# Kernel optimization log

Measured on AMD Instinct MI355X. Metric: run time of the kernel, lower is better.

The kernel has to match this reference:

```python
import jax, jax.numpy as jnp
import numpy as np

N_CELL, N_WELL = 200000, 2000
E_CC, E_CW = 1200000, 200000
CF, WF, H = 16, 8, 128
NUM_PHASES, OUT_SEQ = 3, 25
OUT = NUM_PHASES * OUT_SEQ  # 75


def setup_inputs() -> dict:
    key = jax.random.key(0)
    ks = jax.random.split(key, 24)
    p = lambda k, shp: jax.random.normal(k, shp, dtype=jnp.float32) * 0.02
    return {
        "cell_x": jax.random.normal(ks[0], (N_CELL, CF), dtype=jnp.float32),
        "well_x": jax.random.normal(ks[1], (N_WELL, WF), dtype=jnp.float32),
        "edge_index_cell": jax.random.randint(ks[2], (2, E_CC), 0, N_CELL),
        "edge_well_src": jax.random.randint(ks[3], (E_CW,), 0, N_CELL),
        "edge_well_dst": jax.random.randint(ks[4], (E_CW,), 0, N_WELL),
        # input projections
        "W_cell": p(ks[5], (CF, H)), "b_cell": jnp.zeros((H,), jnp.float32),
        "W_well": p(ks[6], (WF, H)), "b_well": jnp.zeros((H,), jnp.float32),
        # SAGEConv cell->cell: lin_l (on aggregated neighbors, has bias), lin_r (on root, no bias)
        "Wl_cc": p(ks[7], (H, H)), "bl_cc": jnp.zeros((H,), jnp.float32),
        "Wr_cc": p(ks[8], (H, H)),
        # SAGEConv cell->well (bipartite)
        "Wl_cw": p(ks[9], (H, H)), "bl_cw": jnp.zeros((H,), jnp.float32),
        "Wr_cw": p(ks[10], (H, H)),
        # well MLP
        "W_m1": p(ks[11], (H, H)), "b_m1": jnp.zeros((H,), jnp.float32),
        "W_m2": p(ks[12], (H, OUT)), "b_m2": jnp.zeros((OUT,), jnp.float32),
    }


def _mean_aggr(msgs, dst, num_segments):
    # PyG 'mean' aggregation: sum per destination / neighbor count; 0 for isolated nodes.
    s = jax.ops.segment_sum(msgs, dst, num_segments=num_segments)
    c = jax.ops.segment_sum(jnp.ones((dst.shape[0], 1), msgs.dtype), dst, num_segments=num_segments)
    return s / jnp.maximum(c, 1.0)


def reference(cell_x, well_x, edge_index_cell, edge_well_src, edge_well_dst,
              W_cell, b_cell, W_well, b_well,
              Wl_cc, bl_cc, Wr_cc, Wl_cw, bl_cw, Wr_cw,
              W_m1, b_m1, W_m2, b_m2):
    cell_h = cell_x @ W_cell + b_cell                      # [N_cell, H]
    well_h = well_x @ W_well + b_well                      # [N_well, H]

    # SAGEConv(cell_h, edge_index_cell): gather source feats, mean-scatter to dst
    src, dst = edge_index_cell[0], edge_index_cell[1]
    agg_c = _mean_aggr(cell_h[src], dst, N_CELL)           # [N_cell, H]
    cell_h = agg_c @ Wl_cc + bl_cc + cell_h @ Wr_cc

    # Bipartite SAGEConv((cell_h, well_h), edge_well): aggregate cells into wells
    agg_w = _mean_aggr(cell_h[edge_well_src], edge_well_dst, N_WELL)  # [N_well, H]
    well_h = agg_w @ Wl_cw + bl_cw + well_h @ Wr_cw

    # well MLP head
    h = jax.nn.relu(well_h @ W_m1 + b_m1)
    out = h @ W_m2 + b_m2                                  # [N_well, 75]
    return out.reshape(-1, NUM_PHASES, OUT_SEQ)            # [N_well, 3, 25]
```

## Files before the change

### kernel.cpp

```cpp
#include <hip/hip_runtime.h>

#define N_CELL 200000
#define N_WELL 2000
#define E_CC   1200000
#define E_CW   200000
#define CF     16
#define WF     8
#define H      128
#define OUTF   75

#define CAP_C  16
#define CAP_W  224
#define OVF_CAP 16384
#define WPB    4

#define BLD_T  307200
#define MKW_T  50176

__device__ __forceinline__ float b2f(unsigned short u) {
    union { unsigned int i; float f; } v; v.i = ((unsigned int)u) << 16; return v.f;
}
__device__ __forceinline__ unsigned short f2b(float f) {
    union { float f; unsigned int i; } v; v.f = f;
    unsigned int i = v.i;
    return (unsigned short)((i + 0x7fffu + ((i >> 16) & 1u)) >> 16);
}
__device__ __forceinline__ float lo16(unsigned int v) { return b2f((unsigned short)(v & 0xffffu)); }
__device__ __forceinline__ float hi16(unsigned int v) { return b2f((unsigned short)(v >> 16)); }
__device__ __forceinline__ float ldf(const void* p, int i, int bf) {
    return bf ? b2f(((const unsigned short*)p)[i]) : ((const float*)p)[i];
}

__global__ __launch_bounds__(256) void k_sniff(const unsigned int* __restrict__ x, int* __restrict__ flag)
{
    __shared__ int cnt[256];
    int t = threadIdx.x;
    unsigned int d = x[t];
    unsigned int e = (d >> 7) & 0xffu;
    cnt[t] = (e >= 110u && e <= 135u) ? 1 : 0;
    __syncthreads();
    for (int o = 128; o > 0; o >>= 1) { if (t < o) cnt[t] += cnt[t + o]; __syncthreads(); }
    if (t == 0) flag[0] = (cnt[0] >= 192) ? 1 : 0;
}

__global__ __launch_bounds__(128) void k_precomp(const void* __restrict__ W_cell,
                                                 const void* __restrict__ b_cell,
                                                 const void* __restrict__ Wl,
                                                 const void* __restrict__ Wr,
                                                 const void* __restrict__ bl,
                                                 const int* __restrict__ flag,
                                                 float* __restrict__ G1, float* __restrict__ G2,
                                                 float* __restrict__ g1v, float* __restrict__ g2v)
{
    int f = threadIdx.x, b = blockIdx.x, bf = flag[0];
    if (b < 16) {
        float s1 = 0.f, s2 = 0.f;
        for (int j = 0; j < H; ++j) {
            float wc = ldf(W_cell, b * H + j, bf);
            s1 += wc * ldf(Wl, j * H + f, bf);
            s2 += wc * ldf(Wr, j * H + f, bf);
        }
        G1[b * H + f] = s1; G2[b * H + f] = s2;
    } else {
        float s1 = 0.f, s2 = 0.f;
        for (int j = 0; j < H; ++j) {
            float bc = ldf(b_cell, j, bf);
            s1 += bc * ldf(Wl, j * H + f, bf);
            s2 += bc * ldf(Wr, j * H + f, bf);
        }
        g1v[f] = s1; g2v[f] = s2 + ldf(bl, f, bf);
    }
}

__global__ __launch_bounds__(128) void k_precomp2(const float* __restrict__ G1, const float* __restrict__ G2,
                                                  const float* __restrict__ g1v, const float* __restrict__ g2v,
                                                  const void* __restrict__ Wl_cw,
                                                  const void* __restrict__ bl_cw,
                                                  const void* __restrict__ Wr_cw,
                                                  const void* __restrict__ W_well,
                                                  const void* __restrict__ b_well,
                                                  const void* __restrict__ Wm1, const void* __restrict__ Wm2,
                                                  const void* __restrict__ bm1, const void* __restrict__ bm2,
                                                  const int* __restrict__ flag,
                                                  float* __restrict__ A1, float* __restrict__ A2,
                                                  float* __restrict__ Bm,
                                                  float* __restrict__ a1, float* __restrict__ a2,
                                                  float* __restrict__ b0,
                                                  float* __restrict__ Wm1f, float* __restrict__ Wm2f,
                                                  float* __restrict__ bm1f, float* __restrict__ bm2f)
{
    int f = threadIdx.x, b = blockIdx.x, bf = flag[0];
    if (b < 16) {
        float s1 = 0.f, s2 = 0.f;
        for (int j = 0; j < H; ++j) {
            float wl = ldf(Wl_cw, j * H + f, bf);
            s1 += G1[b * H + j] * wl;
            s2 += G2[b * H + j] * wl;
        }
        A1[b * H + f] = s1; A2[b * H + f] = s2;
    } else if (b < 24) {
        int k = b - 16;
        float s = 0.f;
        for (int j = 0; j < H; ++j)
            s += ldf(W_well, k * H + j, bf) * ldf(Wr_cw, j * H + f, bf);
        Bm[k * H + f] = s;
    } else if (b == 24) {
        float s1 = 0.f, s2 = 0.f, s3 = 0.f;
        for (int j = 0; j < H; ++j) {
            float wl = ldf(Wl_cw, j * H + f, bf);
            s1 += g1v[j] * wl;
            s2 += g2v[j] * wl;
            s3 += ldf(b_well, j, bf) * ldf(Wr_cw, j * H + f, bf);
        }
        a1[f] = s1; a2[f] = s2; b0[f] = s3 + ldf(bl_cw, f, bf);
    } else {
        int i = (b - 25) * 128 + f;
        if (i < H * H) Wm1f[i] = ldf(Wm1, i, bf);
        else if (i < H * H + H * OUTF) Wm2f[i - H * H] = ldf(Wm2, i - H * H, bf);
        else if (i < H * H + H * OUTF + H) bm1f[i - H * H - H * OUTF] = ldf(bm1, i - H * H - H * OUTF, bf);
        else if (i < H * H + H * OUTF + H + OUTF) bm2f[i - H * H - H * OUTF - H] = ldf(bm2, i - H * H - H * OUTF - H, bf);
    }
}

__global__ __launch_bounds__(256) void k_markw(const int* __restrict__ ews, const int* __restrict__ ewd,
                                               unsigned char* __restrict__ mark,
                                               int* __restrict__ counts_w, int* __restrict__ buckets_w)
{
    int i = blockIdx.x * 256 + threadIdx.x;
#pragma unroll
    for (int u = 0; u < 4; ++u) {
        int e = i + u * MKW_T;
        if (e < E_CW) {
            unsigned c = (unsigned)ews[e];
            if (c < N_CELL) mark[c] = 1;
            unsigned d = (unsigned)ewd[e];
            if (d < N_WELL) {
                int s = atomicAdd(&counts_w[d], 1);
                if (s < CAP_W) buckets_w[d * CAP_W + s] = (int)c;
            }
        }
    }
}

__global__ __launch_bounds__(256) void k_build(const int* __restrict__ cc_src, const int* __restrict__ cc_dst,
                                               const unsigned char* __restrict__ mark,
                                               int* __restrict__ counts_c,
                                               int* __restrict__ buckets_c,
                                               int* __restrict__ ovf_cnt, int2* __restrict__ ovf)
{
    int i = blockIdx.x * 256 + threadIdx.x;
    int e0 = i, e1 = i + BLD_T, e2 = i + 2 * BLD_T, e3 = i + 3 * BLD_T;
    unsigned d0 = (e0 < E_CC) ? (unsigned)cc_dst[e0] : 0xFFFFFFFFu;
    unsigned d1 = (e1 < E_CC) ? (unsigned)cc_dst[e1] : 0xFFFFFFFFu;
    unsigned d2 = (e2 < E_CC) ? (unsigned)cc_dst[e2] : 0xFFFFFFFFu;
    unsigned d3 = (e3 < E_CC) ? (unsigned)cc_dst[e3] : 0xFFFFFFFFu;
    bool m0 = (d0 < N_CELL) && mark[d0];
    bool m1 = (d1 < N_CELL) && mark[d1];
    bool m2 = (d2 < N_CELL) && mark[d2];
    bool m3 = (d3 < N_CELL) && mark[d3];
    int s0 = m0 ? cc_src[e0] : 0;
    int s1 = m1 ? cc_src[e1] : 0;
    int s2 = m2 ? cc_src[e2] : 0;
    int s3 = m3 ? cc_src[e3] : 0;
    if (m0) {
        int p = atomicAdd(&counts_c[d0], 1);
        if (p < CAP_C) buckets_c[d0 * CAP_C + p] = s0;
        else { int q = atomicAdd(ovf_cnt, 1); if (q < OVF_CAP) { ovf[q].x = (int)d0; ovf[q].y = s0; } }
    }
    if (m1) {
        int p = atomicAdd(&counts_c[d1], 1);
        if (p < CAP_C) buckets_c[d1 * CAP_C + p] = s1;
        else { int q = atomicAdd(ovf_cnt, 1); if (q < OVF_CAP) { ovf[q].x = (int)d1; ovf[q].y = s1; } }
    }
    if (m2) {
        int p = atomicAdd(&counts_c[d2], 1);
        if (p < CAP_C) buckets_c[d2 * CAP_C + p] = s2;
        else { int q = atomicAdd(ovf_cnt, 1); if (q < OVF_CAP) { ovf[q].x = (int)d2; ovf[q].y = s2; } }
    }
    if (m3) {
        int p = atomicAdd(&counts_c[d3], 1);
        if (p < CAP_C) buckets_c[d3 * CAP_C + p] = s3;
        else { int q = atomicAdd(ovf_cnt, 1); if (q < OVF_CAP) { ovf[q].x = (int)d3; ovf[q].y = s3; } }
    }
}

__global__ __launch_bounds__(256) void k_aggA(const void* __restrict__ xr,
                                              const int* __restrict__ flag,
                                              const unsigned char* __restrict__ mark,
                                              const int* __restrict__ counts_c,
                                              const int* __restrict__ buckets_c,
                                              float* __restrict__ y)
{
    int gid = (blockIdx.x * 256 + threadIdx.x) >> 3;
    int jl = threadIdx.x & 7;
    if (gid >= N_CELL) return;
    if (!mark[gid]) return;
    int bf = flag[0];
    int cnt = counts_c[gid]; if (cnt < 0) cnt = 0;
    int lim = (cnt < CAP_C) ? cnt : CAP_C;
    float acc[16];
#pragma unroll
    for (int k = 0; k < 16; ++k) acc[k] = 0.f;

    int j0 = jl, j1 = jl + 8;
    unsigned s0 = (j0 < lim) ? (unsigned)buckets_c[gid * CAP_C + j0] : 0xFFFFFFFFu;
    unsigned s1 = (j1 < lim) ? (unsigned)buckets_c[gid * CAP_C + j1] : 0xFFFFFFFFu;
    if (s0 >= N_CELL) s0 = 0xFFFFFFFFu;
    if (s1 >= N_CELL) s1 = 0xFFFFFFFFu;

    if (bf) {
        uint4 a0, b0q, a1, b1q;
        bool v0 = (s0 != 0xFFFFFFFFu), v1 = (s1 != 0xFFFFFFFFu);
        if (v0) { a0 = ((const uint4*)xr)[(size_t)s0 * 2]; b0q = ((const uint4*)xr)[(size_t)s0 * 2 + 1]; }
        if (v1) { a1 = ((const uint4*)xr)[(size_t)s1 * 2]; b1q = ((const uint4*)xr)[(size_t)s1 * 2 + 1]; }
        if (v0) {
            acc[0] += lo16(a0.x);  acc[1] += hi16(a0.x);
            acc[2] += lo16(a0.y);  acc[3] += hi16(a0.y);
            acc[4] += lo16(a0.z);  acc[5] += hi16(a0.z);
            acc[6] += lo16(a0.w);  acc[7] += hi16(a0.w);
            acc[8] += lo16(b0q.x); acc[9] += hi16(b0q.x);
            acc[10] += lo16(b0q.y); acc[11] += hi16(b0q.y);
            acc[12] += lo16(b0q.z); acc[13] += hi16(b0q.z);
            acc[14] += lo16(b0q.w); acc[15] += hi16(b0q.w);
        }
        if (v1) {
            acc[0] += lo16(a1.x);  acc[1] += hi16(a1.x);
            acc[2] += lo16(a1.y);  acc[3] += hi16(a1.y);
            acc[4] += lo16(a1.z);  acc[5] += hi16(a1.z);
            acc[6] += lo16(a1.w);  acc[7] += hi16(a1.w);
            acc[8] += lo16(b1q.x); acc[9] += hi16(b1q.x);
            acc[10] += lo16(b1q.y); acc[11] += hi16(b1q.y);
            acc[12] += lo16(b1q.z); acc[13] += hi16(b1q.z);
            acc[14] += lo16(b1q.w); acc[15] += hi16(b1q.w);
        }
    } else {
        if (s0 != 0xFFFFFFFFu) {
            const float4* p = (const float4*)xr + (size_t)s0 * 4;
#pragma unroll
            for (int q = 0; q < 4; ++q) {
                float4 v = p[q];
                acc[4 * q] += v.x; acc[4 * q + 1] += v.y; acc[4 * q + 2] += v.z; acc[4 * q + 3] += v.w;
            }
        }
        if (s1 != 0xFFFFFFFFu) {
            const float4* p = (const float4*)xr + (size_t)s1 * 4;
#pragma unroll
            for (int q = 0; q < 4; ++q) {
                float4 v = p[q];
                acc[4 * q] += v.x; acc[4 * q + 1] += v.y; acc[4 * q + 2] += v.z; acc[4 * q + 3] += v.w;
            }
        }
    }
#pragma unroll
    for (int m = 1; m < 8; m <<= 1) {
#pragma unroll
        for (int k = 0; k < 16; ++k) acc[k] += __shfl_xor(acc[k], m, 64);
    }
    float sc = (cnt > 0) ? (1.0f / (float)cnt) : 0.0f;
    float2 st; st.x = acc[2 * jl] * sc; st.y = acc[2 * jl + 1] * sc;
    ((float2*)y)[(size_t)gid * 8 + jl] = st;
}

__global__ __launch_bounds__(256) void k_ovf(const void* __restrict__ xr,
                                             const int* __restrict__ flag,
                                             const int* __restrict__ ovf_cnt,
                                             const int2* __restrict__ ovf,
                                             const int* __restrict__ counts_c,
                                             float* __restrict__ y)
{
    int gid = (blockIdx.x * 256 + threadIdx.x) >> 3;
    int jl = threadIdx.x & 7;
    int n = ovf_cnt[0]; if (n > OVF_CAP) n = OVF_CAP;
    if (gid >= n) return;
    int bf = flag[0];
    unsigned d = (unsigned)ovf[gid].x; if (d >= N_CELL) d = 0;
    unsigned s = (unsigned)ovf[gid].y; if (s >= N_CELL) s = 0;
    int cnt = counts_c[d];
    float inv = (cnt > 0) ? (1.0f / (float)cnt) : 0.0f;
    float v0, v1;
    if (bf) {
        unsigned int u = ((const unsigned int*)xr)[(size_t)s * 8 + jl];
        v0 = lo16(u); v1 = hi16(u);
    } else {
        v0 = ((const float*)xr)[(size_t)s * 16 + 2 * jl];
        v1 = ((const float*)xr)[(size_t)s * 16 + 2 * jl + 1];
    }
    atomicAdd(&y[(size_t)d * 16 + 2 * jl], v0 * inv);
    atomicAdd(&y[(size_t)d * 16 + 2 * jl + 1], v1 * inv);
}

__global__ __launch_bounds__(256) void k_wellagg(const void* __restrict__ xr,
                                                 const int* __restrict__ flag,
                                                 const float* __restrict__ y,
                                                 const int* __restrict__ counts_c,
                                                 const int* __restrict__ counts_w,
                                                 const int* __restrict__ buckets_w,
                                                 const void* __restrict__ wx,
                                                 const float* __restrict__ A1, const float* __restrict__ A2,
                                                 const float* __restrict__ Bm,
                                                 const float* __restrict__ a1, const float* __restrict__ a2,
                                                 const float* __restrict__ b0,
                                                 float* __restrict__ Z)
{
    __shared__ float sP[16], sR[16], sq[1];
    int w = blockIdx.x, t = threadIdx.x, bf = flag[0];
    int g = t >> 3, jl = t & 7;
    if (t < 16) { sP[t] = 0.f; sR[t] = 0.f; }
    if (t == 16) sq[0] = 0.f;
    __syncthreads();

    int cntw = counts_w[w]; if (cntw < 0) cntw = 0;
    int lim = (cntw < CAP_W) ? cntw : CAP_W;

    float p0 = 0.f, p1 = 0.f, r0 = 0.f, r1 = 0.f, qn = 0.f;
    const unsigned int* x32 = (const unsigned int*)xr;
    const float* xf = (const float*)xr;

    for (int e = g; e < lim; e += 32) {
        unsigned c = (unsigned)buckets_w[w * CAP_W + e]; if (c >= N_CELL) c = 0;
        float2 yv = ((const float2*)y)[(size_t)c * 8 + jl];
        p0 += yv.x; p1 += yv.y;
        if (bf) {
            unsigned int u = x32[(size_t)c * 8 + jl];
            r0 += lo16(u); r1 += hi16(u);
        } else {
            r0 += xf[(size_t)c * 16 + 2 * jl];
            r1 += xf[(size_t)c * 16 + 2 * jl + 1];
        }
        if (jl == 0) qn += (counts_c[c] > 0) ? 1.0f : 0.0f;
    }
    atomicAdd(&sP[2 * jl], p0);
    atomicAdd(&sP[2 * jl + 1], p1);
    atomicAdd(&sR[2 * jl], r0);
    atomicAdd(&sR[2 * jl + 1], r1);
    if (jl == 0 && qn != 0.f) atomicAdd(&sq[0], qn);
    __syncthreads();

    int f = t;
    if (f < H) {
        float inv = (cntw > 0) ? (1.0f / (float)cntw) : 0.0f;
        float mask = (cntw > 0) ? 1.0f : 0.0f;
        float wh = (sq[0] * inv) * a1[f] + a2[f];
#pragma unroll
        for (int k = 0; k < 16; ++k)
            wh += (sP[k] * inv) * A1[k * H + f] + (sR[k] * inv) * A2[k * H + f];
        wh *= mask;
        wh += b0[f];
#pragma unroll
        for (int k = 0; k < WF; ++k)
            wh += ldf(wx, w * WF + k, bf) * Bm[k * H + f];
        Z[(size_t)w * H + f] = wh;
    }
}

__global__ __launch_bounds__(128) void k_head(const float* __restrict__ Z,
                                              const float* __restrict__ Wm1f, const float* __restrict__ Wm2f,
                                              const float* __restrict__ bm1f, const float* __restrict__ bm2f,
                                              const int* __restrict__ flag,
                                              void* __restrict__ outp)
{
    __shared__ float sz[WPB][H], sh[WPB][H];
    int w0 = blockIdx.x * WPB, t = threadIdx.x, bf = flag[0];
    float4 zv = ((const float4*)(Z + (size_t)w0 * H))[t];
    ((float4*)&sz[0][0])[t] = zv;
    __syncthreads();

    float acc[WPB];
#pragma unroll
    for (int i = 0; i < WPB; ++i) acc[i] = bm1f[t];
    for (int k = 0; k < H; ++k) {
        float wm = Wm1f[k * H + t];
#pragma unroll
        for (int i = 0; i < WPB; ++i) acc[i] += sz[i][k] * wm;
    }
#pragma unroll
    for (int i = 0; i < WPB; ++i) sh[i][t] = fmaxf(acc[i], 0.f);
    __syncthreads();

    if (t < OUTF) {
        float o[WPB];
#pragma unroll
        for (int i = 0; i < WPB; ++i) o[i] = bm2f[t];
        for (int k = 0; k < H; ++k) {
            float wm = Wm2f[k * OUTF + t];
#pragma unroll
            for (int i = 0; i < WPB; ++i) o[i] += sh[i][k] * wm;
        }
        if (bf) {
#pragma unroll
            for (int i = 0; i < WPB; ++i)
                ((unsigned short*)outp)[(size_t)(w0 + i) * OUTF + t] = f2b(o[i]);
        } else {
#pragma unroll
            for (int i = 0; i < WPB; ++i)
                ((float*)outp)[(size_t)(w0 + i) * OUTF + t] = o[i];
        }
    }
}

extern "C" void kernel_launch(void* const* d_in, const int* in_sizes, int n_in,
                              void* d_out, int out_size, void* d_ws, size_t ws_size,
                              hipStream_t stream)
{
    const void* cell_x = d_in[0];
    const void* well_x = d_in[1];
    const int* eic = (const int*)d_in[2];
    const int* ews = (const int*)d_in[3];
    const int* ewd = (const int*)d_in[4];
    const void* W_cell = d_in[5];
    const void* b_cell = d_in[6];
    const void* W_well = d_in[7];
    const void* b_well = d_in[8];
    const void* Wl_cc = d_in[9];
    const void* bl_cc = d_in[10];
    const void* Wr_cc = d_in[11];
    const void* Wl_cw = d_in[12];
    const void* bl_cw = d_in[13];
    const void* Wr_cw = d_in[14];
    const void* W_m1 = d_in[15];
    const void* b_m1 = d_in[16];
    const void* W_m2 = d_in[17];
    const void* b_m2 = d_in[18];
    (void)in_sizes; (void)n_in; (void)out_size; (void)ws_size;

    const int* cc_src = eic;
    const int* cc_dst = eic + E_CC;

    char* wsp = (char*)d_ws;
    size_t off = 0;
    auto carve = [&](size_t bytes) -> char* {
        char* p = wsp + off;
        off = (off + bytes + 255) & ~(size_t)255;
        return p;
    };

    float* G1   = (float*)carve(16 * H * 4);
    float* G2   = (float*)carve(16 * H * 4);
    float* g1v  = (float*)carve(H * 4);
    float* g2v  = (float*)carve(H * 4);
    float* A1   = (float*)carve(16 * H * 4);
    float* A2   = (float*)carve(16 * H * 4);
    float* Bm   = (float*)carve(WF * H * 4);
    float* a1   = (float*)carve(H * 4);
    float* a2   = (float*)carve(H * 4);
    float* b0   = (float*)carve(H * 4);
    float* Wm1f = (float*)carve(H * H * 4);
    float* Wm2f = (float*)carve(H * OUTF * 4);
    float* bm1f = (float*)carve(H * 4);
    float* bm2f = (float*)carve(OUTF * 4);
    int*   flag = (int*)carve(256);
    size_t zero_beg = off;
    int*   counts   = (int*)carve((size_t)(N_CELL + N_WELL) * 4);
    int*   counts_c = counts;
    int*   counts_w = counts + N_CELL;
    unsigned char* mark = (unsigned char*)carve((size_t)N_CELL);
    int*   ovf_cnt  = (int*)carve(256);
    size_t zero_end = off;
    int*   buckets_c = (int*)carve((size_t)N_CELL * CAP_C * 4);
    int*   buckets_w = (int*)carve((size_t)N_WELL * CAP_W * 4);
    float* y         = (float*)carve((size_t)N_CELL * 16 * 4);
    int2*  ovf       = (int2*)carve((size_t)OVF_CAP * 8);
    float* Z         = (float*)carve((size_t)N_WELL * H * 4);

    k_sniff<<<1, 256, 0, stream>>>((const unsigned int*)cell_x, flag);
    hipMemsetAsync((char*)d_ws + zero_beg, 0, zero_end - zero_beg, stream);
    k_precomp<<<17, 128, 0, stream>>>(W_cell, b_cell, Wl_cc, Wr_cc, bl_cc, flag, G1, G2, g1v, g2v);
    k_precomp2<<<230, 128, 0, stream>>>(G1, G2, g1v, g2v, Wl_cw, bl_cw, Wr_cw, W_well, b_well,
                                        W_m1, W_m2, b_m1, b_m2, flag,
                                        A1, A2, Bm, a1, a2, b0, Wm1f, Wm2f, bm1f, bm2f);
    k_markw<<<MKW_T / 256, 256, 0, stream>>>(ews, ewd, mark, counts_w, buckets_w);
    k_build<<<BLD_T / 256, 256, 0, stream>>>(cc_src, cc_dst, mark, counts_c, buckets_c, ovf_cnt, ovf);
    k_aggA<<<(N_CELL * 8 + 255) / 256, 256, 0, stream>>>(cell_x, flag, mark, counts_c, buckets_c, y);
    k_ovf<<<(OVF_CAP * 8 + 255) / 256, 256, 0, stream>>>(cell_x, flag, ovf_cnt, ovf, counts_c, y);
    k_wellagg<<<N_WELL, 256, 0, stream>>>(cell_x, flag, y, counts_c, counts_w, buckets_w,
                                          well_x, A1, A2, Bm, a1, a2, b0, Z);
    k_head<<<N_WELL / WPB, 128, 0, stream>>>(Z, Wm1f, Wm2f, bm1f, bm2f, flag, d_out);
}
```

Before: 295.4 us.

## Fuse sniff, memset and precompute into one setup kernel; simplify markw and aggA

Merges the dtype-sniff kernel, the workspace memset and the first weight-precompute kernel into a single launch. Each compute block re-sniffs the dtype locally and extra blocks zero the counters with a strided loop, which removes two launches and a serial dependency. k_markw drops its 4-way unroll and uses one thread per edge. k_aggA replaces its two fixed neighbor slots with a loop over bucket entries, which trades explicit load batching for simpler code.

```diff
diff --git a/kernel.cpp b/kernel.cpp
--- a/kernel.cpp
+++ b/kernel.cpp
@@ -15,7 +15,6 @@
 #define WPB    4
 
 #define BLD_T  307200
-#define MKW_T  50176
 
 __device__ __forceinline__ float b2f(unsigned short u) {
     union { unsigned int i; float f; } v; v.i = ((unsigned int)u) << 16; return v.f;
@@ -31,29 +30,34 @@
     return bf ? b2f(((const unsigned short*)p)[i]) : ((const float*)p)[i];
 }
 
-__global__ __launch_bounds__(256) void k_sniff(const unsigned int* __restrict__ x, int* __restrict__ flag)
-{
-    __shared__ int cnt[256];
+__device__ __forceinline__ int sniff128(const unsigned int* __restrict__ x)
+{
+    __shared__ int cnt[128];
     int t = threadIdx.x;
-    unsigned int d = x[t];
-    unsigned int e = (d >> 7) & 0xffu;
-    cnt[t] = (e >= 110u && e <= 135u) ? 1 : 0;
-    __syncthreads();
-    for (int o = 128; o > 0; o >>= 1) { if (t < o) cnt[t] += cnt[t + o]; __syncthreads(); }
-    if (t == 0) flag[0] = (cnt[0] >= 192) ? 1 : 0;
-}
-
-__global__ __launch_bounds__(128) void k_precomp(const void* __restrict__ W_cell,
-                                                 const void* __restrict__ b_cell,
-                                                 const void* __restrict__ Wl,
-                                                 const void* __restrict__ Wr,
-                                                 const void* __restrict__ bl,
-                                                 const int* __restrict__ flag,
-                                                 float* __restrict__ G1, float* __restrict__ G2,
-                                                 float* __restrict__ g1v, float* __restrict__ g2v)
-{
-    int f = threadIdx.x, b = blockIdx.x, bf = flag[0];
+    unsigned a = x[t], b = x[t + 128];
+    unsigned ea = (a >> 7) & 0xffu, eb = (b >> 7) & 0xffu;
+    cnt[t] = ((ea >= 110u && ea <= 135u) ? 1 : 0) + ((eb >= 110u && eb <= 135u) ? 1 : 0);
+    __syncthreads();
+    for (int o = 64; o > 0; o >>= 1) { if (t < o) cnt[t] += cnt[t + o]; __syncthreads(); }
+    int r = (cnt[0] >= 192) ? 1 : 0;
+    __syncthreads();
+    return r;
+}
+
+__global__ __launch_bounds__(128) void k_setup1(const unsigned int* __restrict__ x256,
+                                                const void* __restrict__ W_cell,
+                                                const void* __restrict__ b_cell,
+                                                const void* __restrict__ Wl,
+                                                const void* __restrict__ Wr,
+                                                const void* __restrict__ bl,
+                                                float* __restrict__ G1, float* __restrict__ G2,
+                                                float* __restrict__ g1v, float* __restrict__ g2v,
+                                                int* __restrict__ flag,
+                                                unsigned int* __restrict__ zero_p, int zero_dw)
+{
+    int f = threadIdx.x, b = blockIdx.x;
     if (b < 16) {
+        int bf = sniff128(x256);
         float s1 = 0.f, s2 = 0.f;
         for (int j = 0; j < H; ++j) {
             float wc = ldf(W_cell, b * H + j, bf);
@@ -61,7 +65,8 @@
             s2 += wc * ldf(Wr, j * H + f, bf);
         }
         G1[b * H + f] = s1; G2[b * H + f] = s2;
-    } else {
+    } else if (b == 16) {
+        int bf = sniff128(x256);
         float s1 = 0.f, s2 = 0.f;
         for (int j = 0; j < H; ++j) {
             float bc = ldf(b_cell, j, bf);
@@ -69,25 +74,31 @@
             s2 += bc * ldf(Wr, j * H + f, bf);
         }
         g1v[f] = s1; g2v[f] = s2 + ldf(bl, f, bf);
-    }
-}
-
-__global__ __launch_bounds__(128) void k_precomp2(const float* __restrict__ G1, const float* __restrict__ G2,
-                                                  const float* __restrict__ g1v, const float* __restrict__ g2v,
-                                                  const void* __restrict__ Wl_cw,
-                                                  const void* __restrict__ bl_cw,
-                                                  const void* __restrict__ Wr_cw,
-                                                  const void* __restrict__ W_well,
-                                                  const void* __restrict__ b_well,
-                                                  const void* __restrict__ Wm1, const void* __restrict__ Wm2,
-                                                  const void* __restrict__ bm1, const void* __restrict__ bm2,
-                                                  const int* __restrict__ flag,
-                                                  float* __restrict__ A1, float* __restrict__ A2,
-                                                  float* __restrict__ Bm,
-                                                  float* __restrict__ a1, float* __restrict__ a2,
-                                                  float* __restrict__ b0,
-                                                  float* __restrict__ Wm1f, float* __restrict__ Wm2f,
-                                                  float* __restrict__ bm1f, float* __restrict__ bm2f)
+    } else if (b == 17) {
+        int bf = sniff128(x256);
+        if (f == 0) flag[0] = bf;
+    } else {
+        for (int i = (b - 18) * 128 + f; i < zero_dw; i += 64 * 128)
+            zero_p[i] = 0u;
+    }
+}
+
+__global__ __launch_bounds__(128) void k_setup2(const float* __restrict__ G1, const float* __restrict__ G2,
+                                                const float* __restrict__ g1v, const float* __restrict__ g2v,
+                                                const void* __restrict__ Wl_cw,
+                                                const void* __restrict__ bl_cw,
+                                                const void* __restrict__ Wr_cw,
+                                                const void* __restrict__ W_well,
+                                                const void* __restrict__ b_well,
+                                                const void* __restrict__ Wm1, const void* __restrict__ Wm2,
+                                                const void* __restrict__ bm1, const void* __restrict__ bm2,
+                                                const int* __restrict__ flag,
+                                                float* __restrict__ A1, float* __restrict__ A2,
+                                                float* __restrict__ Bm,
+                                                float* __restrict__ a1, float* __restrict__ a2,
+                                                float* __restrict__ b0,
+                                                float* __restrict__ Wm1f, float* __restrict__ Wm2f,
+                                                float* __restrict__ bm1f, float* __restrict__ bm2f)
 {
     int f = threadIdx.x, b = blockIdx.x, bf = flag[0];
     if (b < 16) {
@@ -122,22 +133,18 @@
     }
 }
 
-__global__ __launch_bounds__(256) void k_markw(const int* __restrict__ ews, const int* __restrict__ ewd,
-                                               unsigned char* __restrict__ mark,
-                                               int* __restrict__ counts_w, int* __restrict__ buckets_w)
+__global__ void k_markw(const int* __restrict__ ews, const int* __restrict__ ewd,
+                        unsigned char* __restrict__ mark,
+                        int* __restrict__ counts_w, int* __restrict__ buckets_w)
 {
     int i = blockIdx.x * 256 + threadIdx.x;
-#pragma unroll
-    for (int u = 0; u < 4; ++u) {
-        int e = i + u * MKW_T;
-        if (e < E_CW) {
-            unsigned c = (unsigned)ews[e];
-            if (c < N_CELL) mark[c] = 1;
-            unsigned d = (unsigned)ewd[e];
-            if (d < N_WELL) {
-                int s = atomicAdd(&counts_w[d], 1);
-                if (s < CAP_W) buckets_w[d * CAP_W + s] = (int)c;
-            }
+    if (i < E_CW) {
+        unsigned c = (unsigned)ews[i];
+        if (c < N_CELL) mark[c] = 1;
+        unsigned d = (unsigned)ewd[i];
+        if (d < N_WELL) {
+            int s = atomicAdd(&counts_w[d], 1);
+            if (s < CAP_W) buckets_w[d * CAP_W + s] = ews[i];
         }
     }
 }
@@ -202,52 +209,26 @@
 #pragma unroll
     for (int k = 0; k < 16; ++k) acc[k] = 0.f;
 
-    int j0 = jl, j1 = jl + 8;
-    unsigned s0 = (j0 < lim) ? (unsigned)buckets_c[gid * CAP_C + j0] : 0xFFFFFFFFu;
-    unsigned s1 = (j1 < lim) ? (unsigned)buckets_c[gid * CAP_C + j1] : 0xFFFFFFFFu;
-    if (s0 >= N_CELL) s0 = 0xFFFFFFFFu;
-    if (s1 >= N_CELL) s1 = 0xFFFFFFFFu;
-
-    if (bf) {
-        uint4 a0, b0q, a1, b1q;
-        bool v0 = (s0 != 0xFFFFFFFFu), v1 = (s1 != 0xFFFFFFFFu);
-        if (v0) { a0 = ((const uint4*)xr)[(size_t)s0 * 2]; b0q = ((const uint4*)xr)[(size_t)s0 * 2 + 1]; }
-        if (v1) { a1 = ((const uint4*)xr)[(size_t)s1 * 2]; b1q = ((const uint4*)xr)[(size_t)s1 * 2 + 1]; }
-        if (v0) {
-            acc[0] += lo16(a0.x);  acc[1] += hi16(a0.x);
-            acc[2] += lo16(a0.y);  acc[3] += hi16(a0.y);
-            acc[4] += lo16(a0.z);  acc[5] += hi16(a0.z);
-            acc[6] += lo16(a0.w);  acc[7] += hi16(a0.w);
-            acc[8] += lo16(b0q.x); acc[9] += hi16(b0q.x);
-            acc[10] += lo16(b0q.y); acc[11] += hi16(b0q.y);
-            acc[12] += lo16(b0q.z); acc[13] += hi16(b0q.z);
-            acc[14] += lo16(b0q.w); acc[15] += hi16(b0q.w);
-        }
-        if (v1) {
-            acc[0] += lo16(a1.x);  acc[1] += hi16(a1.x);
-            acc[2] += lo16(a1.y);  acc[3] += hi16(a1.y);
-            acc[4] += lo16(a1.z);  acc[5] += hi16(a1.z);
-            acc[6] += lo16(a1.w);  acc[7] += hi16(a1.w);
-            acc[8] += lo16(b1q.x); acc[9] += hi16(b1q.x);
-            acc[10] += lo16(b1q.y); acc[11] += hi16(b1q.y);
-            acc[12] += lo16(b1q.z); acc[13] += hi16(b1q.z);
-            acc[14] += lo16(b1q.w); acc[15] += hi16(b1q.w);
-        }
-    } else {
-        if (s0 != 0xFFFFFFFFu) {
-            const float4* p = (const float4*)xr + (size_t)s0 * 4;
+    for (int j = jl; j < lim; j += 8) {
+        unsigned s = (unsigned)buckets_c[gid * CAP_C + j]; if (s >= N_CELL) s = 0;
+        if (bf) {
+            uint4 a = ((const uint4*)xr)[(size_t)s * 2];
+            uint4 b = ((const uint4*)xr)[(size_t)s * 2 + 1];
+            acc[0] += lo16(a.x);  acc[1] += hi16(a.x);
+            acc[2] += lo16(a.y);  acc[3] += hi16(a.y);
+            acc[4] += lo16(a.z);  acc[5] += hi16(a.z);
+            acc[6] += lo16(a.w);  acc[7] += hi16(a.w);
+            acc[8] += lo16(b.x);  acc[9] += hi16(b.x);
+            acc[10] += lo16(b.y); acc[11] += hi16(b.y);
+            acc[12] += lo16(b.z); acc[13] += hi16(b.z);
+            acc[14] += lo16(b.w); acc[15] += hi16(b.w);
+        } else {
+            const float4* p = (const float4*)xr + (size_t)s * 4;
 #pragma unroll
             for (int q = 0; q < 4; ++q) {
                 float4 v = p[q];
-                acc[4 * q] += v.x; acc[4 * q + 1] += v.y; acc[4 * q + 2] += v.z; acc[4 * q + 3] += v.w;
-            }
-        }
-        if (s1 != 0xFFFFFFFFu) {
-            const float4* p = (const float4*)xr + (size_t)s1 * 4;
-#pragma unroll
-            for (int q = 0; q < 4; ++q) {
-                float4 v = p[q];
-                acc[4 * q] += v.x; acc[4 * q + 1] += v.y; acc[4 * q + 2] += v.z; acc[4 * q + 3] += v.w;
+                acc[4 * q]     += v.x; acc[4 * q + 1] += v.y;
+                acc[4 * q + 2] += v.z; acc[4 * q + 3] += v.w;
             }
         }
     }
@@ -462,13 +443,15 @@
     int2*  ovf       = (int2*)carve((size_t)OVF_CAP * 8);
     float* Z         = (float*)carve((size_t)N_WELL * H * 4);
 
-    k_sniff<<<1, 256, 0, stream>>>((const unsigned int*)cell_x, flag);
-    hipMemsetAsync((char*)d_ws + zero_beg, 0, zero_end - zero_beg, stream);
-    k_precomp<<<17, 128, 0, stream>>>(W_cell, b_cell, Wl_cc, Wr_cc, bl_cc, flag, G1, G2, g1v, g2v);
-    k_precomp2<<<230, 128, 0, stream>>>(G1, G2, g1v, g2v, Wl_cw, bl_cw, Wr_cw, W_well, b_well,
-                                        W_m1, W_m2, b_m1, b_m2, flag,
-                                        A1, A2, Bm, a1, a2, b0, Wm1f, Wm2f, bm1f, bm2f);
-    k_markw<<<MKW_T / 256, 256, 0, stream>>>(ews, ewd, mark, counts_w, buckets_w);
+    int zero_dw = (int)((zero_end - zero_beg) / 4);
+
+    k_setup1<<<82, 128, 0, stream>>>((const unsigned int*)cell_x, W_cell, b_cell, Wl_cc, Wr_cc, bl_cc,
+                                     G1, G2, g1v, g2v, flag,
+                                     (unsigned int*)((char*)d_ws + zero_beg), zero_dw);
+    k_setup2<<<230, 128, 0, stream>>>(G1, G2, g1v, g2v, Wl_cw, bl_cw, Wr_cw, W_well, b_well,
+                                      W_m1, W_m2, b_m1, b_m2, flag,
+                                      A1, A2, Bm, a1, a2, b0, Wm1f, Wm2f, bm1f, bm2f);
+    k_markw<<<(E_CW + 255) / 256, 256, 0, stream>>>(ews, ewd, mark, counts_w, buckets_w);
     k_build<<<BLD_T / 256, 256, 0, stream>>>(cc_src, cc_dst, mark, counts_c, buckets_c, ovf_cnt, ovf);
     k_aggA<<<(N_CELL * 8 + 255) / 256, 256, 0, stream>>>(cell_x, flag, mark, counts_c, buckets_c, y);
     k_ovf<<<(OVF_CAP * 8 + 255) / 256, 256, 0, stream>>>(cell_x, flag, ovf_cnt, ovf, counts_c, y);
```

Result: no change. 289.7 us (-1.9%).
